# Performance work log

Measured on AMD Instinct MI355X. Metric: run time of the kernel, lower is better.

Reference implementation:

```python
import jax, jax.numpy as jnp
import numpy as np

LN_EPS = 1e-5

def setup_inputs() -> dict:
    key = jax.random.key(0)
    ks = jax.random.split(key, 12)
    B, T, R, Ds = 4, 128, 64, 128
    N = 2048
    d_id = 128
    max_neurons, max_regions, max_eids = 2048, 128, 256
    U = jax.random.normal(ks[0], (B, T, R, Ds), dtype=jnp.float32)
    neuron_regions = jax.random.randint(ks[1], (B, N), 0, max_regions, dtype=jnp.int32)
    eids = jax.random.randint(ks[2], (B,), 0, max_eids, dtype=jnp.int32)
    r_map = jax.random.randint(ks[3], (max_regions,), 0, R, dtype=jnp.int32)
    s = 0.02
    neuron_slot = jax.random.normal(ks[4], (max_neurons, d_id), dtype=jnp.float32) * s
    region_emb = jax.random.normal(ks[5], (max_regions, d_id), dtype=jnp.float32) * s
    eid_emb = jax.random.normal(ks[6], (max_eids, d_id), dtype=jnp.float32) * s
    ln_gamma = jnp.ones((d_id,), dtype=jnp.float32)
    ln_beta = jnp.zeros((d_id,), dtype=jnp.float32)
    W1 = jax.random.normal(ks[7], (d_id, 2 * Ds), dtype=jnp.float32) * (1.0 / np.sqrt(d_id))
    b1 = jnp.zeros((2 * Ds,), dtype=jnp.float32)
    W2 = jax.random.normal(ks[8], (2 * Ds, Ds + 1), dtype=jnp.float32) * (1.0 / np.sqrt(2 * Ds))
    b2 = jnp.zeros((Ds + 1,), dtype=jnp.float32)  # nn.init.zeros_ on hyper[-1].bias
    return {"U": U, "neuron_regions": neuron_regions, "eids": eids, "r_map": r_map,
            "neuron_slot": neuron_slot, "region_emb": region_emb, "eid_emb": eid_emb,
            "ln_gamma": ln_gamma, "ln_beta": ln_beta, "W1": W1, "b1": b1, "W2": W2, "b2": b2}


def reference(U, neuron_regions, eids, r_map, neuron_slot, region_emb, eid_emb,
              ln_gamma, ln_beta, W1, b1, W2, b2):
    B, T, R, Ds = U.shape
    N = neuron_regions.shape[1]
    # neuron identity embedding: slot + region (+ eid)
    nr = jnp.clip(neuron_regions, 0, region_emb.shape[0] - 1)
    e = neuron_slot[:N][None, :, :] + region_emb[nr]                      # [B,N,d_id]
    e = e + eid_emb[jnp.clip(eids, 0, eid_emb.shape[0] - 1)][:, None, :]
    # hyper-MLP: LayerNorm -> Linear -> GELU(exact) -> Linear
    mu = e.mean(-1, keepdims=True)
    var = ((e - mu) ** 2).mean(-1, keepdims=True)
    h = (e - mu) * jax.lax.rsqrt(var + LN_EPS) * ln_gamma + ln_beta
    h = jax.nn.gelu(h @ W1 + b1, approximate=False)
    wb = h @ W2 + b2                                                      # [B,N,Ds+1]
    w = wb[..., :Ds]                                                      # [B,N,Ds]
    bias = wb[..., Ds]                                                    # [B,N]
    # region-indexed gather + weighted reduce
    local_r = r_map[jnp.clip(neuron_regions, 0, r_map.shape[0] - 1)]      # [B,N]
    lr_safe = jnp.clip(local_r, 0, None)
    idx = jnp.broadcast_to(lr_safe[:, None, :, None], (B, T, N, Ds))
    U_neur = jnp.take_along_axis(U, idx, axis=2)                          # [B,T,N,Ds]
    pred = jnp.einsum('btnd,bnd->btn', U_neur, w) + bias[:, None, :]
    pred = jnp.where((local_r < 0)[:, None, :], jnp.zeros_like(pred), pred)
    return pred
```

## Files before the change

kernel.cpp:

```cpp
#include <hip/hip_runtime.h>
#include <hip/hip_bf16.h>
#include <math.h>

#define DEV __device__ __forceinline__

typedef __attribute__((ext_vector_type(8))) short short8v;
typedef __attribute__((ext_vector_type(4))) float f32x4;

DEV float bf2f(unsigned short u) { return __uint_as_float(((unsigned)u) << 16); }
DEV unsigned short f2bf(float x) {
    unsigned u = __float_as_uint(x);
    return (unsigned short)((u + 0x7fffu + ((u >> 16) & 1u)) >> 16);
}
DEV unsigned pack2(float lo, float hi) {
    return ((unsigned)f2bf(hi) << 16) | (unsigned)f2bf(lo);
}
DEV f32x4 mfma16(short8v a, short8v b, f32x4 c) {
    return __builtin_amdgcn_mfma_f32_16x16x32_bf16(a, b, c, 0, 0, 0);
}

#define NN 2048

__global__ __launch_bounds__(256, 1) void prep_kernel(
    const float* __restrict__ W1, const float* __restrict__ W2,
    const int* __restrict__ r_map, const int* __restrict__ neuron_regions,
    unsigned short* __restrict__ W1T, unsigned short* __restrict__ W2T,
    float* __restrict__ w2col, int* __restrict__ order, int* __restrict__ offs)
{
    __shared__ __align__(16) float T[32][33];
    __shared__ int hist[65], starts[66], cursor[65];
    const int tid = threadIdx.x;
    const int bid = blockIdx.x;

    if (bid < 32) {
        const int tr = bid >> 3, tc = bid & 7;
#pragma unroll
        for (int p = 0; p < 4; p++) {
            const int i = p * 8 + (tid >> 5), j = tid & 31;
            T[i][j] = W1[(tr * 32 + i) * 256 + tc * 32 + j];
        }
        __syncthreads();
#pragma unroll
        for (int p = 0; p < 4; p++) {
            const int i = p * 8 + (tid >> 5), j = tid & 31;
            W1T[(tc * 32 + i) * 128 + tr * 32 + j] = f2bf(T[j][i]);
        }
    } else if (bid < 64) {
        const int bb = bid - 32, tr = bb >> 2, tc = bb & 3;
#pragma unroll
        for (int p = 0; p < 4; p++) {
            const int i = p * 8 + (tid >> 5), j = tid & 31;
            T[i][j] = W2[(tr * 32 + i) * 129 + tc * 32 + j];
        }
        __syncthreads();
#pragma unroll
        for (int p = 0; p < 4; p++) {
            const int i = p * 8 + (tid >> 5), j = tid & 31;
            W2T[(tc * 32 + i) * 256 + tr * 32 + j] = f2bf(T[j][i]);
        }
    } else if (bid == 64) {
        w2col[tid] = W2[tid * 129 + 128];
    } else {
        const int b = bid - 65;
        for (int i = tid; i < 65; i += 256) hist[i] = 0;
        __syncthreads();
        for (int n = tid; n < NN; n += 256) {
            int nr = min(max(neuron_regions[b * NN + n], 0), 127);
            int lr = r_map[nr];
            int bin = (lr < 0) ? 64 : min(lr, 63);
            atomicAdd(&hist[bin], 1);
        }
        __syncthreads();
        if (tid == 0) {
            int run = 0;
            for (int i = 0; i < 65; i++) { starts[i] = run; cursor[i] = run; run += hist[i]; }
            starts[65] = run;
        }
        __syncthreads();
        for (int i = tid; i < 66; i += 256) offs[b * 66 + i] = starts[i];
        for (int n = tid; n < NN; n += 256) {
            int nr = min(max(neuron_regions[b * NN + n], 0), 127);
            int lr = r_map[nr];
            int bin = (lr < 0) ? 64 : min(lr, 63);
            int pos = atomicAdd(&cursor[bin], 1);
            order[b * NN + pos] = n;
        }
    }
}

__global__ __launch_bounds__(256, 1) void p1_kernel(
    const int* __restrict__ neuron_regions, const int* __restrict__ eids,
    const float* __restrict__ neuron_slot, const float* __restrict__ region_emb,
    const float* __restrict__ eid_emb, const float* __restrict__ ln_gamma,
    const float* __restrict__ ln_beta, const float* __restrict__ b1,
    const float* __restrict__ b2, const unsigned short* __restrict__ W1T,
    const unsigned short* __restrict__ W2T, const float* __restrict__ w2col,
    unsigned short* __restrict__ w_ws, float* __restrict__ bias_ws)
{
    __shared__ __align__(16) unsigned short hT[16][136];
    __shared__ __align__(16) unsigned short H1[16][264];
    __shared__ float biasp[16];
    const int tid = threadIdx.x;
    const int row0 = blockIdx.x * 16;
    if (tid < 16) biasp[tid] = 0.f;

    {
        const int rr = tid >> 4, q = tid & 15;
        const int row = row0 + rr;
        const int b = row >> 11, n = row & (NN - 1);
        int nr = min(max(neuron_regions[b * NN + n], 0), 127);
        int eid = min(max(eids[b], 0), 255);
        const float* ns = neuron_slot + n * 128 + q * 8;
        const float* re = region_emb + nr * 128 + q * 8;
        const float* ee = eid_emb + eid * 128 + q * 8;
        float e[8];
        {
            float4 a0 = *(const float4*)ns, a1 = *(const float4*)(ns + 4);
            float4 c0 = *(const float4*)re, c1 = *(const float4*)(re + 4);
            float4 d0 = *(const float4*)ee, d1 = *(const float4*)(ee + 4);
            e[0] = a0.x + c0.x + d0.x; e[1] = a0.y + c0.y + d0.y;
            e[2] = a0.z + c0.z + d0.z; e[3] = a0.w + c0.w + d0.w;
            e[4] = a1.x + c1.x + d1.x; e[5] = a1.y + c1.y + d1.y;
            e[6] = a1.z + c1.z + d1.z; e[7] = a1.w + c1.w + d1.w;
        }
        float s = 0.f, s2 = 0.f;
#pragma unroll
        for (int i = 0; i < 8; i++) { s += e[i]; s2 += e[i] * e[i]; }
        s += __shfl_xor(s, 1);  s2 += __shfl_xor(s2, 1);
        s += __shfl_xor(s, 2);  s2 += __shfl_xor(s2, 2);
        s += __shfl_xor(s, 4);  s2 += __shfl_xor(s2, 4);
        s += __shfl_xor(s, 8);  s2 += __shfl_xor(s2, 8);
        const float mu = s * (1.f / 128.f);
        const float var = s2 * (1.f / 128.f) - mu * mu;
        const float rstd = rsqrtf(var + 1e-5f);
        float4 g0 = *(const float4*)(ln_gamma + q * 8), g1 = *(const float4*)(ln_gamma + q * 8 + 4);
        float4 t0 = *(const float4*)(ln_beta + q * 8),  t1 = *(const float4*)(ln_beta + q * 8 + 4);
        float gm[8] = {g0.x, g0.y, g0.z, g0.w, g1.x, g1.y, g1.z, g1.w};
        float bt[8] = {t0.x, t0.y, t0.z, t0.w, t1.x, t1.y, t1.z, t1.w};
        float h[8];
#pragma unroll
        for (int i = 0; i < 8; i++) h[i] = (e[i] - mu) * rstd * gm[i] + bt[i];
        uint4 pk;
        pk.x = pack2(h[0], h[1]); pk.y = pack2(h[2], h[3]);
        pk.z = pack2(h[4], h[5]); pk.w = pack2(h[6], h[7]);
        *(uint4*)&hT[rr][q * 8] = pk;
    }
    __syncthreads();

    const int wv = tid >> 6, l = tid & 63;
    const int lr = l & 15, lh = l >> 4;

    short8v afr[4];
#pragma unroll
    for (int ks = 0; ks < 4; ks++)
        afr[ks] = *(const short8v*)&hT[lr][ks * 32 + lh * 8];

    f32x4 acc1[4];
    short8v bfr[4][4];
    float w2c[4];
#pragma unroll
    for (int nt = 0; nt < 4; nt++) {
        const int n = wv * 64 + nt * 16 + lr;
#pragma unroll
        for (int ks = 0; ks < 4; ks++)
            bfr[nt][ks] = *(const short8v*)(W1T + n * 128 + ks * 32 + lh * 8);
        const float bb = b1[n];
        acc1[nt].x = bb; acc1[nt].y = bb; acc1[nt].z = bb; acc1[nt].w = bb;
        w2c[nt] = w2col[n];
    }
#pragma unroll
    for (int nt = 0; nt < 4; nt++)
#pragma unroll
        for (int ks = 0; ks < 4; ks++)
            acc1[nt] = mfma16(afr[ks], bfr[nt][ks], acc1[nt]);

    float pb[4] = {0.f, 0.f, 0.f, 0.f};
#pragma unroll
    for (int nt = 0; nt < 4; nt++) {
        const int n = wv * 64 + nt * 16 + lr;
#pragma unroll
        for (int j = 0; j < 4; j++) {
            const float x = acc1[nt][j];
            const float g = 0.5f * x * (1.f + erff(x * 0.70710678118654752f));
            H1[lh * 4 + j][n] = f2bf(g);
            pb[j] += g * w2c[nt];
        }
    }
#pragma unroll
    for (int j = 0; j < 4; j++) {
        pb[j] += __shfl_xor(pb[j], 1);
        pb[j] += __shfl_xor(pb[j], 2);
        pb[j] += __shfl_xor(pb[j], 4);
        pb[j] += __shfl_xor(pb[j], 8);
    }
    if (lr == 0) {
#pragma unroll
        for (int j = 0; j < 4; j++) atomicAdd(&biasp[lh * 4 + j], pb[j]);
    }
    __syncthreads();

    if (tid < 16) bias_ws[row0 + tid] = biasp[tid] + b2[128];

    short8v a2[8];
#pragma unroll
    for (int ks = 0; ks < 8; ks++)
        a2[ks] = *(const short8v*)&H1[lr][ks * 32 + lh * 8];

    f32x4 acc2[2];
    short8v b2f[2][8];
#pragma unroll
    for (int nt = 0; nt < 2; nt++) {
        const int n = wv * 32 + nt * 16 + lr;
#pragma unroll
        for (int ks = 0; ks < 8; ks++)
            b2f[nt][ks] = *(const short8v*)(W2T + n * 256 + ks * 32 + lh * 8);
        const float bb = b2[n];
        acc2[nt].x = bb; acc2[nt].y = bb; acc2[nt].z = bb; acc2[nt].w = bb;
    }
#pragma unroll
    for (int nt = 0; nt < 2; nt++)
#pragma unroll
        for (int ks = 0; ks < 8; ks++)
            acc2[nt] = mfma16(a2[ks], b2f[nt][ks], acc2[nt]);

#pragma unroll
    for (int nt = 0; nt < 2; nt++) {
        const int n = wv * 32 + nt * 16 + lr;
#pragma unroll
        for (int j = 0; j < 4; j++)
            hT[lh * 4 + j][n] = f2bf(acc2[nt][j]);
    }
    __syncthreads();
    {
        const int r = tid >> 4, c = tid & 15;
        uint4 v = *(const uint4*)&hT[r][c * 8];
        *(uint4*)(w_ws + (row0 + r) * 128 + c * 8) = v;
    }
}

__global__ __launch_bounds__(256, 1) void p2_kernel(
    const float* __restrict__ U, const int* __restrict__ order,
    const int* __restrict__ offs, const unsigned short* __restrict__ w_ws,
    const float* __restrict__ bias_ws, float* __restrict__ out)
{
    __shared__ __align__(16) unsigned short Ubf[128][136];
    __shared__ __align__(16) unsigned short Bt[32][136];
    __shared__ int nidS[32];
    __shared__ float biasS[32];
    const int tid = threadIdx.x;
    const int bid = blockIdx.x;

    if (bid >= 256) {
        const int b = bid - 256;
        const int s64 = offs[b * 66 + 64], s65 = offs[b * 66 + 65];
        const int cnt = s65 - s64;
        for (int idx = tid; idx < cnt * 128; idx += 256) {
            const int j = idx >> 7, t = idx & 127;
            const int n = order[b * NN + s64 + j];
            out[(b * 128 + t) * NN + n] = 0.f;
        }
        return;
    }

    const int b = bid >> 6, slot = bid & 63;
    const int s0 = offs[b * 66 + slot], s1 = offs[b * 66 + slot + 1];
    const int cnt = s1 - s0;
    if (cnt <= 0) return;

    {
        const int t = tid >> 1, half = tid & 1;
        const float* src = U + ((size_t)((b * 128 + t) * 64 + slot)) * 128 + half * 64;
        unsigned short* dst = &Ubf[t][half * 64];
#pragma unroll
        for (int j = 0; j < 16; j++) {
            float4 v = ((const float4*)src)[j];
            ((uint2*)dst)[j] = make_uint2(pack2(v.x, v.y), pack2(v.z, v.w));
        }
    }
    __syncthreads();

    const int wv = tid >> 6, l = tid & 63;
    const int lr = l & 15, lh = l >> 4;

    short8v afr[2][4];
#pragma unroll
    for (int mt = 0; mt < 2; mt++)
#pragma unroll
        for (int ks = 0; ks < 4; ks++)
            afr[mt][ks] = *(const short8v*)&Ubf[wv * 32 + mt * 16 + lr][ks * 32 + lh * 8];

    const int nChunks = (cnt + 31) >> 5;
    for (int c = 0; c < nChunks; c++) {
        const int base = s0 + c * 32;
        const int cc = min(cnt - c * 32, 32);
        __syncthreads();
        if (tid < 32) {
            const int nid = (tid < cc) ? order[b * NN + base + tid] : -1;
            nidS[tid] = nid;
            biasS[tid] = (nid >= 0) ? bias_ws[b * NN + nid] : 0.f;
        }
        {
            const int jj = tid >> 3, q = tid & 7;
            const int nid = (jj < cc) ? order[b * NN + base + jj] : -1;
            unsigned short* dst = &Bt[jj][q * 16];
            if (nid >= 0) {
                const uint4* src = (const uint4*)(w_ws + ((size_t)(b * NN + nid)) * 128 + q * 16);
                ((uint4*)dst)[0] = src[0];
                ((uint4*)dst)[1] = src[1];
            } else {
                ((uint4*)dst)[0] = make_uint4(0, 0, 0, 0);
                ((uint4*)dst)[1] = make_uint4(0, 0, 0, 0);
            }
        }
        __syncthreads();

        f32x4 acc[2][2];
#pragma unroll
        for (int mt = 0; mt < 2; mt++)
#pragma unroll
            for (int nt = 0; nt < 2; nt++) {
                acc[mt][nt].x = 0.f; acc[mt][nt].y = 0.f;
                acc[mt][nt].z = 0.f; acc[mt][nt].w = 0.f;
            }
        short8v bfr[2][4];
#pragma unroll
        for (int nt = 0; nt < 2; nt++)
#pragma unroll
            for (int ks = 0; ks < 4; ks++)
                bfr[nt][ks] = *(const short8v*)&Bt[nt * 16 + lr][ks * 32 + lh * 8];
#pragma unroll
        for (int mt = 0; mt < 2; mt++)
#pragma unroll
            for (int nt = 0; nt < 2; nt++)
#pragma unroll
                for (int ks = 0; ks < 4; ks++)
                    acc[mt][nt] = mfma16(afr[mt][ks], bfr[nt][ks], acc[mt][nt]);

#pragma unroll
        for (int nt = 0; nt < 2; nt++) {
            const int j = nt * 16 + lr;
            const int nid = nidS[j];
            if (nid >= 0) {
                const float bs = biasS[j];
#pragma unroll
                for (int mt = 0; mt < 2; mt++) {
                    const int tt = wv * 32 + mt * 16 + lh * 4;
#pragma unroll
                    for (int jr = 0; jr < 4; jr++)
                        out[(b * 128 + tt + jr) * NN + nid] = acc[mt][nt][jr] + bs;
                }
            }
        }
    }
}

extern "C" void kernel_launch(void* const* d_in, const int* in_sizes, int n_in,
                              void* d_out, int out_size, void* d_ws, size_t ws_size,
                              hipStream_t stream)
{
    const float* U              = (const float*)d_in[0];
    const int*   neuron_regions = (const int*)d_in[1];
    const int*   eids           = (const int*)d_in[2];
    const int*   r_map          = (const int*)d_in[3];
    const float* neuron_slot    = (const float*)d_in[4];
    const float* region_emb     = (const float*)d_in[5];
    const float* eid_emb        = (const float*)d_in[6];
    const float* ln_gamma       = (const float*)d_in[7];
    const float* ln_beta        = (const float*)d_in[8];
    const float* W1             = (const float*)d_in[9];
    const float* b1             = (const float*)d_in[10];
    const float* W2             = (const float*)d_in[11];
    const float* b2             = (const float*)d_in[12];

    char* ws = (char*)d_ws;
    unsigned short* w_ws  = (unsigned short*)(ws);
    float*          bias_ws = (float*)(ws + 2097152);
    unsigned short* W1T   = (unsigned short*)(ws + 2129920);
    unsigned short* W2T   = (unsigned short*)(ws + 2195456);
    float*          w2col = (float*)(ws + 2260992);
    int*            order = (int*)(ws + 2262016);
    int*            offs  = (int*)(ws + 2294784);
    float* outp = (float*)d_out;

    hipLaunchKernelGGL(prep_kernel, dim3(69), dim3(256), 0, stream,
                       W1, W2, r_map, neuron_regions, W1T, W2T, w2col, order, offs);
    hipLaunchKernelGGL(p1_kernel, dim3(512), dim3(256), 0, stream,
                       neuron_regions, eids, neuron_slot, region_emb, eid_emb,
                       ln_gamma, ln_beta, b1, b2, W1T, W2T, w2col, w_ws, bias_ws);
    hipLaunchKernelGGL(p2_kernel, dim3(260), dim3(256), 0, stream,
                       U, order, offs, w_ws, bias_ws, outp);
}
```

Measured before the change: 41.84 us.

## Stage predictions in sorted order and scatter with a coalesced transpose kernel

p2 previously wrote output with scattered 4-byte stores at neuron-indexed columns. It now writes predictions contiguously into a sorted-order staging buffer. A new p3 kernel uses an inverse permutation (jinv, built in prep) to gather rows and write the output with coalesced float4 stores, and it also handles the zeroing of masked neurons. The p1 MFMA loops are reordered to interleave loads and MMAs per tile, which cuts register pressure. The cost is an extra 4 MB round trip through the workspace and one more kernel launch, and p3 uses only 64 blocks.

Result: slower. 43.03 us (+2.8%).

```diff
diff --git a/kernel.cpp b/kernel.cpp
--- a/kernel.cpp
+++ b/kernel.cpp
@@ -25,7 +25,8 @@
     const float* __restrict__ W1, const float* __restrict__ W2,
     const int* __restrict__ r_map, const int* __restrict__ neuron_regions,
     unsigned short* __restrict__ W1T, unsigned short* __restrict__ W2T,
-    float* __restrict__ w2col, int* __restrict__ order, int* __restrict__ offs)
+    float* __restrict__ w2col, int* __restrict__ order, int* __restrict__ offs,
+    int* __restrict__ jinv)
 {
     __shared__ __align__(16) float T[32][33];
     __shared__ int hist[65], starts[66], cursor[65];
@@ -84,6 +85,7 @@
             int bin = (lr < 0) ? 64 : min(lr, 63);
             int pos = atomicAdd(&cursor[bin], 1);
             order[b * NN + pos] = n;
+            jinv[b * NN + n] = (bin == 64) ? -1 : pos;
         }
     }
 }
@@ -156,23 +158,21 @@
         afr[ks] = *(const short8v*)&hT[lr][ks * 32 + lh * 8];
 
     f32x4 acc1[4];
-    short8v bfr[4][4];
     float w2c[4];
 #pragma unroll
     for (int nt = 0; nt < 4; nt++) {
         const int n = wv * 64 + nt * 16 + lr;
+        short8v bfr[4];
 #pragma unroll
         for (int ks = 0; ks < 4; ks++)
-            bfr[nt][ks] = *(const short8v*)(W1T + n * 128 + ks * 32 + lh * 8);
+            bfr[ks] = *(const short8v*)(W1T + n * 128 + ks * 32 + lh * 8);
         const float bb = b1[n];
-        acc1[nt].x = bb; acc1[nt].y = bb; acc1[nt].z = bb; acc1[nt].w = bb;
+        f32x4 a; a.x = bb; a.y = bb; a.z = bb; a.w = bb;
+#pragma unroll
+        for (int ks = 0; ks < 4; ks++) a = mfma16(afr[ks], bfr[ks], a);
+        acc1[nt] = a;
         w2c[nt] = w2col[n];
     }
-#pragma unroll
-    for (int nt = 0; nt < 4; nt++)
-#pragma unroll
-        for (int ks = 0; ks < 4; ks++)
-            acc1[nt] = mfma16(afr[ks], bfr[nt][ks], acc1[nt]);
 
     float pb[4] = {0.f, 0.f, 0.f, 0.f};
 #pragma unroll
@@ -207,21 +207,19 @@
         a2[ks] = *(const short8v*)&H1[lr][ks * 32 + lh * 8];
 
     f32x4 acc2[2];
-    short8v b2f[2][8];
 #pragma unroll
     for (int nt = 0; nt < 2; nt++) {
         const int n = wv * 32 + nt * 16 + lr;
+        short8v bf[8];
 #pragma unroll
         for (int ks = 0; ks < 8; ks++)
-            b2f[nt][ks] = *(const short8v*)(W2T + n * 256 + ks * 32 + lh * 8);
+            bf[ks] = *(const short8v*)(W2T + n * 256 + ks * 32 + lh * 8);
         const float bb = b2[n];
-        acc2[nt].x = bb; acc2[nt].y = bb; acc2[nt].z = bb; acc2[nt].w = bb;
-    }
-#pragma unroll
-    for (int nt = 0; nt < 2; nt++)
-#pragma unroll
-        for (int ks = 0; ks < 8; ks++)
-            acc2[nt] = mfma16(a2[ks], b2f[nt][ks], acc2[nt]);
+        f32x4 a; a.x = bb; a.y = bb; a.z = bb; a.w = bb;
+#pragma unroll
+        for (int ks = 0; ks < 8; ks++) a = mfma16(a2[ks], bf[ks], a);
+        acc2[nt] = a;
+    }
 
 #pragma unroll
     for (int nt = 0; nt < 2; nt++) {
@@ -241,26 +239,13 @@
 __global__ __launch_bounds__(256, 1) void p2_kernel(
     const float* __restrict__ U, const int* __restrict__ order,
     const int* __restrict__ offs, const unsigned short* __restrict__ w_ws,
-    const float* __restrict__ bias_ws, float* __restrict__ out)
+    const float* __restrict__ bias_ws, float* __restrict__ predS)
 {
     __shared__ __align__(16) unsigned short Ubf[128][136];
     __shared__ __align__(16) unsigned short Bt[32][136];
-    __shared__ int nidS[32];
     __shared__ float biasS[32];
     const int tid = threadIdx.x;
     const int bid = blockIdx.x;
-
-    if (bid >= 256) {
-        const int b = bid - 256;
-        const int s64 = offs[b * 66 + 64], s65 = offs[b * 66 + 65];
-        const int cnt = s65 - s64;
-        for (int idx = tid; idx < cnt * 128; idx += 256) {
-            const int j = idx >> 7, t = idx & 127;
-            const int n = order[b * NN + s64 + j];
-            out[(b * 128 + t) * NN + n] = 0.f;
-        }
-        return;
-    }
 
     const int b = bid >> 6, slot = bid & 63;
     const int s0 = offs[b * 66 + slot], s1 = offs[b * 66 + slot + 1];
@@ -296,7 +281,6 @@
         __syncthreads();
         if (tid < 32) {
             const int nid = (tid < cc) ? order[b * NN + base + tid] : -1;
-            nidS[tid] = nid;
             biasS[tid] = (nid >= 0) ? bias_ws[b * NN + nid] : 0.f;
         }
         {
@@ -314,6 +298,13 @@
         }
         __syncthreads();
 
+        short8v bfr[2][4];
+#pragma unroll
+        for (int nt = 0; nt < 2; nt++)
+#pragma unroll
+            for (int ks = 0; ks < 4; ks++)
+                bfr[nt][ks] = *(const short8v*)&Bt[nt * 16 + lr][ks * 32 + lh * 8];
+
         f32x4 acc[2][2];
 #pragma unroll
         for (int mt = 0; mt < 2; mt++)
@@ -322,12 +313,6 @@
                 acc[mt][nt].x = 0.f; acc[mt][nt].y = 0.f;
                 acc[mt][nt].z = 0.f; acc[mt][nt].w = 0.f;
             }
-        short8v bfr[2][4];
-#pragma unroll
-        for (int nt = 0; nt < 2; nt++)
-#pragma unroll
-            for (int ks = 0; ks < 4; ks++)
-                bfr[nt][ks] = *(const short8v*)&Bt[nt * 16 + lr][ks * 32 + lh * 8];
 #pragma unroll
         for (int mt = 0; mt < 2; mt++)
 #pragma unroll
@@ -339,18 +324,57 @@
 #pragma unroll
         for (int nt = 0; nt < 2; nt++) {
             const int j = nt * 16 + lr;
-            const int nid = nidS[j];
-            if (nid >= 0) {
+            if (j < cc) {
                 const float bs = biasS[j];
 #pragma unroll
                 for (int mt = 0; mt < 2; mt++) {
-                    const int tt = wv * 32 + mt * 16 + lh * 4;
-#pragma unroll
-                    for (int jr = 0; jr < 4; jr++)
-                        out[(b * 128 + tt + jr) * NN + nid] = acc[mt][nt][jr] + bs;
+                    float4 o;
+                    o.x = acc[mt][nt][0] + bs; o.y = acc[mt][nt][1] + bs;
+                    o.z = acc[mt][nt][2] + bs; o.w = acc[mt][nt][3] + bs;
+                    float* dst = predS + ((size_t)(b * NN + base + j)) * 128
+                               + wv * 32 + mt * 16 + lh * 4;
+                    *(float4*)dst = o;
                 }
             }
         }
+    }
+}
+
+__global__ __launch_bounds__(256, 1) void p3_kernel(
+    const float* __restrict__ predS, const int* __restrict__ jinv,
+    float* __restrict__ out)
+{
+    const int tid = threadIdx.x;
+    const int bid = blockIdx.x;
+    const int b = bid >> 4, tg = bid & 15;
+    const int t0 = tg * 8;
+    const int n0 = tid * 8;
+
+    int jv[8];
+    *(int4*)&jv[0] = *(const int4*)(jinv + b * NN + n0);
+    *(int4*)&jv[4] = *(const int4*)(jinv + b * NN + n0 + 4);
+
+    float v[8][8];
+#pragma unroll
+    for (int i = 0; i < 8; i++) {
+        if (jv[i] >= 0) {
+            const float* src = predS + ((size_t)(b * NN + jv[i])) * 128 + t0;
+            float4 a = *(const float4*)src, c = *(const float4*)(src + 4);
+            v[i][0] = a.x; v[i][1] = a.y; v[i][2] = a.z; v[i][3] = a.w;
+            v[i][4] = c.x; v[i][5] = c.y; v[i][6] = c.z; v[i][7] = c.w;
+        } else {
+#pragma unroll
+            for (int t = 0; t < 8; t++) v[i][t] = 0.f;
+        }
+    }
+#pragma unroll
+    for (int t = 0; t < 8; t++) {
+        float4 o0, o1;
+        o0.x = v[0][t]; o0.y = v[1][t]; o0.z = v[2][t]; o0.w = v[3][t];
+        o1.x = v[4][t]; o1.y = v[5][t]; o1.z = v[6][t]; o1.w = v[7][t];
+        float* dst = out + ((size_t)(b * 128 + t0 + t)) * NN + n0;
+        ((float4*)dst)[0] = o0;
+        ((float4*)dst)[1] = o1;
     }
 }
 
@@ -373,20 +397,24 @@
     const float* b2             = (const float*)d_in[12];
 
     char* ws = (char*)d_ws;
-    unsigned short* w_ws  = (unsigned short*)(ws);
-    float*          bias_ws = (float*)(ws + 2097152);
-    unsigned short* W1T   = (unsigned short*)(ws + 2129920);
-    unsigned short* W2T   = (unsigned short*)(ws + 2195456);
-    float*          w2col = (float*)(ws + 2260992);
-    int*            order = (int*)(ws + 2262016);
-    int*            offs  = (int*)(ws + 2294784);
+    unsigned short* w_ws    = (unsigned short*)(ws);
+    float*          bias_ws = (float*)(ws + 0x200000);
+    unsigned short* W1T     = (unsigned short*)(ws + 0x208000);
+    unsigned short* W2T     = (unsigned short*)(ws + 0x218000);
+    float*          w2col   = (float*)(ws + 0x228000);
+    int*            order   = (int*)(ws + 0x228400);
+    int*            offs    = (int*)(ws + 0x230400);
+    int*            jinv    = (int*)(ws + 0x230C00);
+    float*          predS   = (float*)(ws + 0x400000);
     float* outp = (float*)d_out;
 
     hipLaunchKernelGGL(prep_kernel, dim3(69), dim3(256), 0, stream,
-                       W1, W2, r_map, neuron_regions, W1T, W2T, w2col, order, offs);
+                       W1, W2, r_map, neuron_regions, W1T, W2T, w2col, order, offs, jinv);
     hipLaunchKernelGGL(p1_kernel, dim3(512), dim3(256), 0, stream,
                        neuron_regions, eids, neuron_slot, region_emb, eid_emb,
                        ln_gamma, ln_beta, b1, b2, W1T, W2T, w2col, w_ws, bias_ws);
-    hipLaunchKernelGGL(p2_kernel, dim3(260), dim3(256), 0, stream,
-                       U, order, offs, w_ws, bias_ws, outp);
-}
+    hipLaunchKernelGGL(p2_kernel, dim3(256), dim3(256), 0, stream,
+                       U, order, offs, w_ws, bias_ws, predS);
+    hipLaunchKernelGGL(p3_kernel, dim3(64), dim3(256), 0, stream,
+                       predS, jinv, outp);
+}
```

## Fuse prep, hyper-MLP and gather-reduce into one persistent kernel with grid barriers

Applied to the files above, without the earlier changes.

Merges the three kernel launches into a single 256-block kernel that uses software grid barriers (atomic counter plus spin) between the weight-transpose, hyper-MLP and gather-reduce phases. Each block builds its own neuron list per region slot in shared memory, replacing the global histogram/order sort, and loads its U tile before the first barrier. The intent is to remove launch gaps and overlap the U load with the weight prep. In exchange it adds a memset, relies on all 256 blocks being co-resident for the spin barriers, and halves MLP parallelism to 32 rows per block.

Measured after the change: 90.56 us. 116% more time.

```diff
diff --git a/kernel.cpp b/kernel.cpp
--- a/kernel.cpp
+++ b/kernel.cpp
@@ -7,7 +7,6 @@
 typedef __attribute__((ext_vector_type(8))) short short8v;
 typedef __attribute__((ext_vector_type(4))) float f32x4;
 
-DEV float bf2f(unsigned short u) { return __uint_as_float(((unsigned)u) << 16); }
 DEV unsigned short f2bf(float x) {
     unsigned u = __float_as_uint(x);
     return (unsigned short)((u + 0x7fffu + ((u >> 16) & 1u)) >> 16);
@@ -21,290 +20,278 @@
 
 #define NN 2048
 
-__global__ __launch_bounds__(256, 1) void prep_kernel(
-    const float* __restrict__ W1, const float* __restrict__ W2,
-    const int* __restrict__ r_map, const int* __restrict__ neuron_regions,
-    unsigned short* __restrict__ W1T, unsigned short* __restrict__ W2T,
-    float* __restrict__ w2col, int* __restrict__ order, int* __restrict__ offs)
+struct __align__(16) Smem {
+    unsigned short Ubf[128][136];
+    int list[2048];
+    unsigned short hT[32][136];
+    union {
+        unsigned short H1[16][264];
+        unsigned short Bt[32][136];
+        float T[32][33];
+        unsigned short bounce[16][136];
+    } u;
+    int rmapS[128];
+    float biasp[32];
+    float biasS[32];
+    int nidS[32];
+    int cnt, deadcnt;
+};
+
+DEV void gridbar(int* ctr, int nb) {
+    __syncthreads();
+    if (threadIdx.x == 0) {
+        __threadfence();
+        __hip_atomic_fetch_add(ctr, 1, __ATOMIC_ACQ_REL, __HIP_MEMORY_SCOPE_AGENT);
+        int guard = 0;
+        while (guard < (1 << 20)) {
+            if (__hip_atomic_load(ctr, __ATOMIC_ACQUIRE, __HIP_MEMORY_SCOPE_AGENT) >= nb)
+                break;
+            __builtin_amdgcn_s_sleep(2);
+            ++guard;
+        }
+        __threadfence();
+    }
+    __syncthreads();
+}
+
+__global__ __launch_bounds__(256, 1) void fused_kernel(
+    const float* __restrict__ U, const int* __restrict__ neuron_regions,
+    const int* __restrict__ eids, const int* __restrict__ r_map,
+    const float* __restrict__ neuron_slot, const float* __restrict__ region_emb,
+    const float* __restrict__ eid_emb, const float* __restrict__ ln_gamma,
+    const float* __restrict__ ln_beta, const float* __restrict__ W1,
+    const float* __restrict__ b1, const float* __restrict__ W2,
+    const float* __restrict__ b2, unsigned short* __restrict__ W1T,
+    unsigned short* __restrict__ W2T, float* __restrict__ w2col,
+    unsigned short* __restrict__ w_ws, float* __restrict__ bias_ws,
+    int* __restrict__ bar, float* __restrict__ out)
 {
-    __shared__ __align__(16) float T[32][33];
-    __shared__ int hist[65], starts[66], cursor[65];
+    __shared__ Smem s;
     const int tid = threadIdx.x;
     const int bid = blockIdx.x;
-
-    if (bid < 32) {
-        const int tr = bid >> 3, tc = bid & 7;
-#pragma unroll
-        for (int p = 0; p < 4; p++) {
-            const int i = p * 8 + (tid >> 5), j = tid & 31;
-            T[i][j] = W1[(tr * 32 + i) * 256 + tc * 32 + j];
-        }
-        __syncthreads();
-#pragma unroll
-        for (int p = 0; p < 4; p++) {
-            const int i = p * 8 + (tid >> 5), j = tid & 31;
-            W1T[(tc * 32 + i) * 128 + tr * 32 + j] = f2bf(T[j][i]);
-        }
-    } else if (bid < 64) {
-        const int bb = bid - 32, tr = bb >> 2, tc = bb & 3;
-#pragma unroll
-        for (int p = 0; p < 4; p++) {
-            const int i = p * 8 + (tid >> 5), j = tid & 31;
-            T[i][j] = W2[(tr * 32 + i) * 129 + tc * 32 + j];
-        }
-        __syncthreads();
-#pragma unroll
-        for (int p = 0; p < 4; p++) {
-            const int i = p * 8 + (tid >> 5), j = tid & 31;
-            W2T[(tc * 32 + i) * 256 + tr * 32 + j] = f2bf(T[j][i]);
-        }
-    } else if (bid == 64) {
-        w2col[tid] = W2[tid * 129 + 128];
-    } else {
-        const int b = bid - 65;
-        for (int i = tid; i < 65; i += 256) hist[i] = 0;
-        __syncthreads();
-        for (int n = tid; n < NN; n += 256) {
-            int nr = min(max(neuron_regions[b * NN + n], 0), 127);
-            int lr = r_map[nr];
-            int bin = (lr < 0) ? 64 : min(lr, 63);
-            atomicAdd(&hist[bin], 1);
-        }
-        __syncthreads();
-        if (tid == 0) {
-            int run = 0;
-            for (int i = 0; i < 65; i++) { starts[i] = run; cursor[i] = run; run += hist[i]; }
-            starts[65] = run;
-        }
-        __syncthreads();
-        for (int i = tid; i < 66; i += 256) offs[b * 66 + i] = starts[i];
-        for (int n = tid; n < NN; n += 256) {
-            int nr = min(max(neuron_regions[b * NN + n], 0), 127);
-            int lr = r_map[nr];
-            int bin = (lr < 0) ? 64 : min(lr, 63);
-            int pos = atomicAdd(&cursor[bin], 1);
-            order[b * NN + pos] = n;
-        }
-    }
-}
-
-__global__ __launch_bounds__(256, 1) void p1_kernel(
-    const int* __restrict__ neuron_regions, const int* __restrict__ eids,
-    const float* __restrict__ neuron_slot, const float* __restrict__ region_emb,
-    const float* __restrict__ eid_emb, const float* __restrict__ ln_gamma,
-    const float* __restrict__ ln_beta, const float* __restrict__ b1,
-    const float* __restrict__ b2, const unsigned short* __restrict__ W1T,
-    const unsigned short* __restrict__ W2T, const float* __restrict__ w2col,
-    unsigned short* __restrict__ w_ws, float* __restrict__ bias_ws)
-{
-    __shared__ __align__(16) unsigned short hT[16][136];
-    __shared__ __align__(16) unsigned short H1[16][264];
-    __shared__ float biasp[16];
-    const int tid = threadIdx.x;
-    const int row0 = blockIdx.x * 16;
-    if (tid < 16) biasp[tid] = 0.f;
-
-    {
-        const int rr = tid >> 4, q = tid & 15;
-        const int row = row0 + rr;
-        const int b = row >> 11, n = row & (NN - 1);
-        int nr = min(max(neuron_regions[b * NN + n], 0), 127);
-        int eid = min(max(eids[b], 0), 255);
-        const float* ns = neuron_slot + n * 128 + q * 8;
-        const float* re = region_emb + nr * 128 + q * 8;
-        const float* ee = eid_emb + eid * 128 + q * 8;
-        float e[8];
-        {
-            float4 a0 = *(const float4*)ns, a1 = *(const float4*)(ns + 4);
-            float4 c0 = *(const float4*)re, c1 = *(const float4*)(re + 4);
-            float4 d0 = *(const float4*)ee, d1 = *(const float4*)(ee + 4);
-            e[0] = a0.x + c0.x + d0.x; e[1] = a0.y + c0.y + d0.y;
-            e[2] = a0.z + c0.z + d0.z; e[3] = a0.w + c0.w + d0.w;
-            e[4] = a1.x + c1.x + d1.x; e[5] = a1.y + c1.y + d1.y;
-            e[6] = a1.z + c1.z + d1.z; e[7] = a1.w + c1.w + d1.w;
-        }
-        float s = 0.f, s2 = 0.f;
-#pragma unroll
-        for (int i = 0; i < 8; i++) { s += e[i]; s2 += e[i] * e[i]; }
-        s += __shfl_xor(s, 1);  s2 += __shfl_xor(s2, 1);
-        s += __shfl_xor(s, 2);  s2 += __shfl_xor(s2, 2);
-        s += __shfl_xor(s, 4);  s2 += __shfl_xor(s2, 4);
-        s += __shfl_xor(s, 8);  s2 += __shfl_xor(s2, 8);
-        const float mu = s * (1.f / 128.f);
-        const float var = s2 * (1.f / 128.f) - mu * mu;
-        const float rstd = rsqrtf(var + 1e-5f);
-        float4 g0 = *(const float4*)(ln_gamma + q * 8), g1 = *(const float4*)(ln_gamma + q * 8 + 4);
-        float4 t0 = *(const float4*)(ln_beta + q * 8),  t1 = *(const float4*)(ln_beta + q * 8 + 4);
-        float gm[8] = {g0.x, g0.y, g0.z, g0.w, g1.x, g1.y, g1.z, g1.w};
-        float bt[8] = {t0.x, t0.y, t0.z, t0.w, t1.x, t1.y, t1.z, t1.w};
-        float h[8];
-#pragma unroll
-        for (int i = 0; i < 8; i++) h[i] = (e[i] - mu) * rstd * gm[i] + bt[i];
-        uint4 pk;
-        pk.x = pack2(h[0], h[1]); pk.y = pack2(h[2], h[3]);
-        pk.z = pack2(h[4], h[5]); pk.w = pack2(h[6], h[7]);
-        *(uint4*)&hT[rr][q * 8] = pk;
-    }
-    __syncthreads();
-
-    const int wv = tid >> 6, l = tid & 63;
-    const int lr = l & 15, lh = l >> 4;
-
-    short8v afr[4];
-#pragma unroll
-    for (int ks = 0; ks < 4; ks++)
-        afr[ks] = *(const short8v*)&hT[lr][ks * 32 + lh * 8];
-
-    f32x4 acc1[4];
-    short8v bfr[4][4];
-    float w2c[4];
-#pragma unroll
-    for (int nt = 0; nt < 4; nt++) {
-        const int n = wv * 64 + nt * 16 + lr;
-#pragma unroll
-        for (int ks = 0; ks < 4; ks++)
-            bfr[nt][ks] = *(const short8v*)(W1T + n * 128 + ks * 32 + lh * 8);
-        const float bb = b1[n];
-        acc1[nt].x = bb; acc1[nt].y = bb; acc1[nt].z = bb; acc1[nt].w = bb;
-        w2c[nt] = w2col[n];
-    }
-#pragma unroll
-    for (int nt = 0; nt < 4; nt++)
-#pragma unroll
-        for (int ks = 0; ks < 4; ks++)
-            acc1[nt] = mfma16(afr[ks], bfr[nt][ks], acc1[nt]);
-
-    float pb[4] = {0.f, 0.f, 0.f, 0.f};
-#pragma unroll
-    for (int nt = 0; nt < 4; nt++) {
-        const int n = wv * 64 + nt * 16 + lr;
-#pragma unroll
-        for (int j = 0; j < 4; j++) {
-            const float x = acc1[nt][j];
-            const float g = 0.5f * x * (1.f + erff(x * 0.70710678118654752f));
-            H1[lh * 4 + j][n] = f2bf(g);
-            pb[j] += g * w2c[nt];
-        }
-    }
-#pragma unroll
-    for (int j = 0; j < 4; j++) {
-        pb[j] += __shfl_xor(pb[j], 1);
-        pb[j] += __shfl_xor(pb[j], 2);
-        pb[j] += __shfl_xor(pb[j], 4);
-        pb[j] += __shfl_xor(pb[j], 8);
-    }
-    if (lr == 0) {
-#pragma unroll
-        for (int j = 0; j < 4; j++) atomicAdd(&biasp[lh * 4 + j], pb[j]);
-    }
-    __syncthreads();
-
-    if (tid < 16) bias_ws[row0 + tid] = biasp[tid] + b2[128];
-
-    short8v a2[8];
-#pragma unroll
-    for (int ks = 0; ks < 8; ks++)
-        a2[ks] = *(const short8v*)&H1[lr][ks * 32 + lh * 8];
-
-    f32x4 acc2[2];
-    short8v b2f[2][8];
-#pragma unroll
-    for (int nt = 0; nt < 2; nt++) {
-        const int n = wv * 32 + nt * 16 + lr;
-#pragma unroll
-        for (int ks = 0; ks < 8; ks++)
-            b2f[nt][ks] = *(const short8v*)(W2T + n * 256 + ks * 32 + lh * 8);
-        const float bb = b2[n];
-        acc2[nt].x = bb; acc2[nt].y = bb; acc2[nt].z = bb; acc2[nt].w = bb;
-    }
-#pragma unroll
-    for (int nt = 0; nt < 2; nt++)
-#pragma unroll
-        for (int ks = 0; ks < 8; ks++)
-            acc2[nt] = mfma16(a2[ks], b2f[nt][ks], acc2[nt]);
-
-#pragma unroll
-    for (int nt = 0; nt < 2; nt++) {
-        const int n = wv * 32 + nt * 16 + lr;
-#pragma unroll
-        for (int j = 0; j < 4; j++)
-            hT[lh * 4 + j][n] = f2bf(acc2[nt][j]);
-    }
-    __syncthreads();
-    {
-        const int r = tid >> 4, c = tid & 15;
-        uint4 v = *(const uint4*)&hT[r][c * 8];
-        *(uint4*)(w_ws + (row0 + r) * 128 + c * 8) = v;
-    }
-}
-
-__global__ __launch_bounds__(256, 1) void p2_kernel(
-    const float* __restrict__ U, const int* __restrict__ order,
-    const int* __restrict__ offs, const unsigned short* __restrict__ w_ws,
-    const float* __restrict__ bias_ws, float* __restrict__ out)
-{
-    __shared__ __align__(16) unsigned short Ubf[128][136];
-    __shared__ __align__(16) unsigned short Bt[32][136];
-    __shared__ int nidS[32];
-    __shared__ float biasS[32];
-    const int tid = threadIdx.x;
-    const int bid = blockIdx.x;
-
-    if (bid >= 256) {
-        const int b = bid - 256;
-        const int s64 = offs[b * 66 + 64], s65 = offs[b * 66 + 65];
-        const int cnt = s65 - s64;
-        for (int idx = tid; idx < cnt * 128; idx += 256) {
-            const int j = idx >> 7, t = idx & 127;
-            const int n = order[b * NN + s64 + j];
-            out[(b * 128 + t) * NN + n] = 0.f;
-        }
-        return;
-    }
-
-    const int b = bid >> 6, slot = bid & 63;
-    const int s0 = offs[b * 66 + slot], s1 = offs[b * 66 + slot + 1];
-    const int cnt = s1 - s0;
-    if (cnt <= 0) return;
+    const int bb2 = bid >> 6, slot = bid & 63;
+
+    if (tid == 0) { s.cnt = 0; s.deadcnt = 0; }
+    if (tid < 32) s.biasp[tid] = 0.f;
+    if (tid < 128) s.rmapS[tid] = r_map[tid];
 
     {
         const int t = tid >> 1, half = tid & 1;
-        const float* src = U + ((size_t)((b * 128 + t) * 64 + slot)) * 128 + half * 64;
-        unsigned short* dst = &Ubf[t][half * 64];
+        const float* src = U + ((size_t)((bb2 * 128 + t) * 64 + slot)) * 128 + half * 64;
+        unsigned short* dst = &s.Ubf[t][half * 64];
 #pragma unroll
         for (int j = 0; j < 16; j++) {
             float4 v = ((const float4*)src)[j];
             ((uint2*)dst)[j] = make_uint2(pack2(v.x, v.y), pack2(v.z, v.w));
         }
     }
+
+    if (bid < 32) {
+        const int tr = bid >> 3, tc = bid & 7;
+#pragma unroll
+        for (int p = 0; p < 4; p++) {
+            const int i = p * 8 + (tid >> 5), j = tid & 31;
+            s.u.T[i][j] = W1[(tr * 32 + i) * 256 + tc * 32 + j];
+        }
+        __syncthreads();
+#pragma unroll
+        for (int p = 0; p < 4; p++) {
+            const int i = p * 8 + (tid >> 5), j = tid & 31;
+            W1T[(tc * 32 + i) * 128 + tr * 32 + j] = f2bf(s.u.T[j][i]);
+        }
+    } else if (bid < 64) {
+        const int bb = bid - 32, tr = bb >> 2, tc = bb & 3;
+#pragma unroll
+        for (int p = 0; p < 4; p++) {
+            const int i = p * 8 + (tid >> 5), j = tid & 31;
+            s.u.T[i][j] = W2[(tr * 32 + i) * 129 + tc * 32 + j];
+        }
+        __syncthreads();
+#pragma unroll
+        for (int p = 0; p < 4; p++) {
+            const int i = p * 8 + (tid >> 5), j = tid & 31;
+            W2T[(tc * 32 + i) * 256 + tr * 32 + j] = f2bf(s.u.T[j][i]);
+        }
+    } else if (bid == 64) {
+        w2col[tid] = W2[tid * 129 + 128];
+    }
     __syncthreads();
+
+    for (int n = tid; n < NN; n += 256) {
+        int reg = min(max(neuron_regions[bb2 * NN + n], 0), 127);
+        int lrv = s.rmapS[reg];
+        if (lrv >= 0) {
+            if (min(lrv, 63) == slot) { int p = atomicAdd(&s.cnt, 1); s.list[p] = n; }
+        } else if (slot == 0) {
+            int p = atomicAdd(&s.deadcnt, 1); s.list[2047 - p] = n;
+        }
+    }
+
+    {
+        const int rr = tid >> 4, q = tid & 15;
+#pragma unroll
+        for (int hh = 0; hh < 2; hh++) {
+            const int row = bid * 32 + hh * 16 + rr;
+            const int bh = row >> 11, n = row & (NN - 1);
+            int nr = min(max(neuron_regions[bh * NN + n], 0), 127);
+            int eid = min(max(eids[bh], 0), 255);
+            const float* ns = neuron_slot + n * 128 + q * 8;
+            const float* re = region_emb + nr * 128 + q * 8;
+            const float* ee = eid_emb + eid * 128 + q * 8;
+            float e[8];
+            {
+                float4 a0 = *(const float4*)ns, a1 = *(const float4*)(ns + 4);
+                float4 c0 = *(const float4*)re, c1 = *(const float4*)(re + 4);
+                float4 d0 = *(const float4*)ee, d1 = *(const float4*)(ee + 4);
+                e[0] = a0.x + c0.x + d0.x; e[1] = a0.y + c0.y + d0.y;
+                e[2] = a0.z + c0.z + d0.z; e[3] = a0.w + c0.w + d0.w;
+                e[4] = a1.x + c1.x + d1.x; e[5] = a1.y + c1.y + d1.y;
+                e[6] = a1.z + c1.z + d1.z; e[7] = a1.w + c1.w + d1.w;
+            }
+            float sm = 0.f, s2 = 0.f;
+#pragma unroll
+            for (int i = 0; i < 8; i++) { sm += e[i]; s2 += e[i] * e[i]; }
+            sm += __shfl_xor(sm, 1); s2 += __shfl_xor(s2, 1);
+            sm += __shfl_xor(sm, 2); s2 += __shfl_xor(s2, 2);
+            sm += __shfl_xor(sm, 4); s2 += __shfl_xor(s2, 4);
+            sm += __shfl_xor(sm, 8); s2 += __shfl_xor(s2, 8);
+            const float mu = sm * (1.f / 128.f);
+            const float var = s2 * (1.f / 128.f) - mu * mu;
+            const float rstd = rsqrtf(var + 1e-5f);
+            float4 g0 = *(const float4*)(ln_gamma + q * 8), g1 = *(const float4*)(ln_gamma + q * 8 + 4);
+            float4 t0 = *(const float4*)(ln_beta + q * 8),  t1 = *(const float4*)(ln_beta + q * 8 + 4);
+            float gm[8] = {g0.x, g0.y, g0.z, g0.w, g1.x, g1.y, g1.z, g1.w};
+            float bt[8] = {t0.x, t0.y, t0.z, t0.w, t1.x, t1.y, t1.z, t1.w};
+            float h[8];
+#pragma unroll
+            for (int i = 0; i < 8; i++) h[i] = (e[i] - mu) * rstd * gm[i] + bt[i];
+            uint4 pk;
+            pk.x = pack2(h[0], h[1]); pk.y = pack2(h[2], h[3]);
+            pk.z = pack2(h[4], h[5]); pk.w = pack2(h[6], h[7]);
+            *(uint4*)&s.hT[hh * 16 + rr][q * 8] = pk;
+        }
+    }
+
+    gridbar(bar + 0, 256);
 
     const int wv = tid >> 6, l = tid & 63;
     const int lr = l & 15, lh = l >> 4;
-
-    short8v afr[2][4];
+    const float b2last = b2[128];
+
+#pragma unroll 1
+    for (int half = 0; half < 2; half++) {
+        const int row0h = bid * 32 + half * 16;
+        short8v afr[4];
+#pragma unroll
+        for (int ks = 0; ks < 4; ks++)
+            afr[ks] = *(const short8v*)&s.hT[half * 16 + lr][ks * 32 + lh * 8];
+
+        f32x4 acc1[4];
+        float w2c[4];
+#pragma unroll
+        for (int nt = 0; nt < 4; nt++) {
+            const int n = wv * 64 + nt * 16 + lr;
+            short8v bfr[4];
+#pragma unroll
+            for (int ks = 0; ks < 4; ks++)
+                bfr[ks] = *(const short8v*)(W1T + n * 128 + ks * 32 + lh * 8);
+            const float bbv = b1[n];
+            f32x4 a; a.x = bbv; a.y = bbv; a.z = bbv; a.w = bbv;
+#pragma unroll
+            for (int ks = 0; ks < 4; ks++) a = mfma16(afr[ks], bfr[ks], a);
+            acc1[nt] = a;
+            w2c[nt] = w2col[n];
+        }
+
+        __syncthreads();
+        float pb[4] = {0.f, 0.f, 0.f, 0.f};
+#pragma unroll
+        for (int nt = 0; nt < 4; nt++) {
+            const int n = wv * 64 + nt * 16 + lr;
+#pragma unroll
+            for (int j = 0; j < 4; j++) {
+                const float x = acc1[nt][j];
+                const float g = 0.5f * x * (1.f + erff(x * 0.70710678118654752f));
+                s.u.H1[lh * 4 + j][n] = f2bf(g);
+                pb[j] += g * w2c[nt];
+            }
+        }
+#pragma unroll
+        for (int j = 0; j < 4; j++) {
+            pb[j] += __shfl_xor(pb[j], 1);
+            pb[j] += __shfl_xor(pb[j], 2);
+            pb[j] += __shfl_xor(pb[j], 4);
+            pb[j] += __shfl_xor(pb[j], 8);
+        }
+        if (lr == 0) {
+#pragma unroll
+            for (int j = 0; j < 4; j++) atomicAdd(&s.biasp[half * 16 + lh * 4 + j], pb[j]);
+        }
+        __syncthreads();
+        if (tid < 16) bias_ws[row0h + tid] = s.biasp[half * 16 + tid] + b2last;
+
+        short8v a2[8];
+#pragma unroll
+        for (int ks = 0; ks < 8; ks++)
+            a2[ks] = *(const short8v*)&s.u.H1[lr][ks * 32 + lh * 8];
+
+        f32x4 acc2[2];
+#pragma unroll
+        for (int nt = 0; nt < 2; nt++) {
+            const int n = wv * 32 + nt * 16 + lr;
+            short8v bf[8];
+#pragma unroll
+            for (int ks = 0; ks < 8; ks++)
+                bf[ks] = *(const short8v*)(W2T + n * 256 + ks * 32 + lh * 8);
+            const float bbv = b2[n];
+            f32x4 a; a.x = bbv; a.y = bbv; a.z = bbv; a.w = bbv;
+#pragma unroll
+            for (int ks = 0; ks < 8; ks++) a = mfma16(a2[ks], bf[ks], a);
+            acc2[nt] = a;
+        }
+
+        __syncthreads();
+#pragma unroll
+        for (int nt = 0; nt < 2; nt++) {
+            const int n = wv * 32 + nt * 16 + lr;
+#pragma unroll
+            for (int j = 0; j < 4; j++)
+                s.u.bounce[lh * 4 + j][n] = f2bf(acc2[nt][j]);
+        }
+        __syncthreads();
+        {
+            const int r = tid >> 4, c = tid & 15;
+            *(uint4*)(w_ws + (size_t)(row0h + r) * 128 + c * 8) = *(const uint4*)&s.u.bounce[r][c * 8];
+        }
+    }
+
+    gridbar(bar + 1, 256);
+
+    const int cnt = s.cnt;
+    short8v afr2[2][4];
 #pragma unroll
     for (int mt = 0; mt < 2; mt++)
 #pragma unroll
         for (int ks = 0; ks < 4; ks++)
-            afr[mt][ks] = *(const short8v*)&Ubf[wv * 32 + mt * 16 + lr][ks * 32 + lh * 8];
+            afr2[mt][ks] = *(const short8v*)&s.Ubf[wv * 32 + mt * 16 + lr][ks * 32 + lh * 8];
 
     const int nChunks = (cnt + 31) >> 5;
+#pragma unroll 1
     for (int c = 0; c < nChunks; c++) {
-        const int base = s0 + c * 32;
-        const int cc = min(cnt - c * 32, 32);
+        const int base = c * 32;
+        const int cc = min(cnt - base, 32);
         __syncthreads();
         if (tid < 32) {
-            const int nid = (tid < cc) ? order[b * NN + base + tid] : -1;
-            nidS[tid] = nid;
-            biasS[tid] = (nid >= 0) ? bias_ws[b * NN + nid] : 0.f;
+            const int nid = (tid < cc) ? s.list[base + tid] : -1;
+            s.nidS[tid] = nid;
+            s.biasS[tid] = (nid >= 0) ? bias_ws[bb2 * NN + nid] : 0.f;
         }
         {
             const int jj = tid >> 3, q = tid & 7;
-            const int nid = (jj < cc) ? order[b * NN + base + jj] : -1;
-            unsigned short* dst = &Bt[jj][q * 16];
+            const int nid = (jj < cc) ? s.list[base + jj] : -1;
+            unsigned short* dst = &s.u.Bt[jj][q * 16];
             if (nid >= 0) {
-                const uint4* src = (const uint4*)(w_ws + ((size_t)(b * NN + nid)) * 128 + q * 16);
+                const uint4* src = (const uint4*)(w_ws + ((size_t)(bb2 * NN + nid)) * 128 + q * 16);
                 ((uint4*)dst)[0] = src[0];
                 ((uint4*)dst)[1] = src[1];
             } else {
@@ -314,6 +301,13 @@
         }
         __syncthreads();
 
+        short8v bfr2[2][4];
+#pragma unroll
+        for (int nt = 0; nt < 2; nt++)
+#pragma unroll
+            for (int ks = 0; ks < 4; ks++)
+                bfr2[nt][ks] = *(const short8v*)&s.u.Bt[nt * 16 + lr][ks * 32 + lh * 8];
+
         f32x4 acc[2][2];
 #pragma unroll
         for (int mt = 0; mt < 2; mt++)
@@ -322,34 +316,37 @@
                 acc[mt][nt].x = 0.f; acc[mt][nt].y = 0.f;
                 acc[mt][nt].z = 0.f; acc[mt][nt].w = 0.f;
             }
-        short8v bfr[2][4];
-#pragma unroll
-        for (int nt = 0; nt < 2; nt++)
-#pragma unroll
-            for (int ks = 0; ks < 4; ks++)
-                bfr[nt][ks] = *(const short8v*)&Bt[nt * 16 + lr][ks * 32 + lh * 8];
 #pragma unroll
         for (int mt = 0; mt < 2; mt++)
 #pragma unroll
             for (int nt = 0; nt < 2; nt++)
 #pragma unroll
                 for (int ks = 0; ks < 4; ks++)
-                    acc[mt][nt] = mfma16(afr[mt][ks], bfr[nt][ks], acc[mt][nt]);
+                    acc[mt][nt] = mfma16(afr2[mt][ks], bfr2[nt][ks], acc[mt][nt]);
 
 #pragma unroll
         for (int nt = 0; nt < 2; nt++) {
             const int j = nt * 16 + lr;
-            const int nid = nidS[j];
+            const int nid = s.nidS[j];
             if (nid >= 0) {
-                const float bs = biasS[j];
+                const float bs = s.biasS[j];
 #pragma unroll
                 for (int mt = 0; mt < 2; mt++) {
                     const int tt = wv * 32 + mt * 16 + lh * 4;
 #pragma unroll
                     for (int jr = 0; jr < 4; jr++)
-                        out[(b * 128 + tt + jr) * NN + nid] = acc[mt][nt][jr] + bs;
+                        out[(size_t)(bb2 * 128 + tt + jr) * NN + nid] = acc[mt][nt][jr] + bs;
                 }
             }
+        }
+    }
+
+    if (slot == 0) {
+        const int dc = s.deadcnt;
+        for (int idx = tid; idx < dc * 128; idx += 256) {
+            const int j = idx >> 7, t = idx & 127;
+            const int n = s.list[2047 - j];
+            out[(size_t)(bb2 * 128 + t) * NN + n] = 0.f;
         }
     }
 }
@@ -373,20 +370,17 @@
     const float* b2             = (const float*)d_in[12];
 
     char* ws = (char*)d_ws;
-    unsigned short* w_ws  = (unsigned short*)(ws);
-    float*          bias_ws = (float*)(ws + 2097152);
-    unsigned short* W1T   = (unsigned short*)(ws + 2129920);
-    unsigned short* W2T   = (unsigned short*)(ws + 2195456);
-    float*          w2col = (float*)(ws + 2260992);
-    int*            order = (int*)(ws + 2262016);
-    int*            offs  = (int*)(ws + 2294784);
+    unsigned short* w_ws    = (unsigned short*)(ws);
+    float*          bias_ws = (float*)(ws + 0x200000);
+    unsigned short* W1T     = (unsigned short*)(ws + 0x208000);
+    unsigned short* W2T     = (unsigned short*)(ws + 0x218000);
+    float*          w2col   = (float*)(ws + 0x228000);
+    int*            bar     = (int*)(ws + 0x600000);
     float* outp = (float*)d_out;
 
-    hipLaunchKernelGGL(prep_kernel, dim3(69), dim3(256), 0, stream,
-                       W1, W2, r_map, neuron_regions, W1T, W2T, w2col, order, offs);
-    hipLaunchKernelGGL(p1_kernel, dim3(512), dim3(256), 0, stream,
-                       neuron_regions, eids, neuron_slot, region_emb, eid_emb,
-                       ln_gamma, ln_beta, b1, b2, W1T, W2T, w2col, w_ws, bias_ws);
-    hipLaunchKernelGGL(p2_kernel, dim3(260), dim3(256), 0, stream,
-                       U, order, offs, w_ws, bias_ws, outp);
-}
+    hipMemsetAsync(bar, 0, 16, stream);
+    hipLaunchKernelGGL(fused_kernel, dim3(256), dim3(256), 0, stream,
+                       U, neuron_regions, eids, r_map, neuron_slot, region_emb,
+                       eid_emb, ln_gamma, ln_beta, W1, b1, W2, b2,
+                       W1T, W2T, w2col, w_ws, bias_ws, bar, outp);
+}
```
